# Optimization experiments

Measured on AMD Instinct MI355X. Metric: run time of the kernel, lower is better.

The kernel has to match this reference:

```python
import jax, jax.numpy as jnp
import numpy as np

N_NODES = 100000
N_EDGES = 3200000
IN_DIM = 512
OUT_DIM = 3


def _sage_conv(x, src, dst, ll_w, ll_b, lr_w):
    # PyG SAGEConv (mean aggr): out = lin_l(mean_{j in N(i)} x_j) + lin_r(x_i)
    n = x.shape[0]
    msgs = x[src]                                            # [E, d_in]
    agg = jax.ops.segment_sum(msgs, dst, num_segments=n)      # [N, d_in]
    cnt = jax.ops.segment_sum(jnp.ones((src.shape[0],), x.dtype), dst, num_segments=n)
    mean = agg / jnp.maximum(cnt, 1.0)[:, None]
    return mean @ ll_w + ll_b + x @ lr_w


def setup_inputs() -> dict:
    key = jax.random.key(0)
    ks = jax.random.split(key, 16)
    d = {}
    d["x"] = jax.random.normal(ks[0], (N_NODES, IN_DIM), dtype=jnp.float32)
    d["edge_index"] = jax.random.randint(ks[1], (2, N_EDGES), 0, N_NODES, dtype=jnp.int64)
    s = lambda fan_in: 1.0 / np.sqrt(fan_in)
    d["fc1_w"] = jax.random.uniform(ks[2], (IN_DIM, 16), jnp.float32, -s(IN_DIM), s(IN_DIM))
    d["fc1_b"] = jax.random.uniform(ks[3], (16,), jnp.float32, -s(IN_DIM), s(IN_DIM))
    d["conv1_ll_w"] = jax.random.uniform(ks[4], (16, 32), jnp.float32, -s(16), s(16))
    d["conv1_ll_b"] = jnp.zeros((32,), jnp.float32)
    d["conv1_lr_w"] = jax.random.uniform(ks[5], (16, 32), jnp.float32, -s(16), s(16))
    d["conv2_ll_w"] = jax.random.uniform(ks[6], (32, 16), jnp.float32, -s(32), s(32))
    d["conv2_ll_b"] = jnp.zeros((16,), jnp.float32)
    d["conv2_lr_w"] = jax.random.uniform(ks[7], (32, 16), jnp.float32, -s(32), s(32))
    d["fc2_w"] = jax.random.uniform(ks[8], (16, OUT_DIM), jnp.float32, -s(16), s(16))
    d["fc2_b"] = jax.random.uniform(ks[9], (OUT_DIM,), jnp.float32, -s(16), s(16))
    return d


def reference(x, edge_index, fc1_w, fc1_b, conv1_ll_w, conv1_ll_b, conv1_lr_w,
              conv2_ll_w, conv2_ll_b, conv2_lr_w, fc2_w, fc2_b):
    src, dst = edge_index[0], edge_index[1]
    h = jax.nn.relu(x @ fc1_w + fc1_b)                              # [N, 16]
    h = jax.nn.relu(_sage_conv(h, src, dst, conv1_ll_w, conv1_ll_b, conv1_lr_w))  # [N, 32]
    h = jax.nn.relu(_sage_conv(h, src, dst, conv2_ll_w, conv2_ll_b, conv2_lr_w))  # [N, 16]
    h = h @ fc2_w + fc2_b                                           # [N, 3]
    gsi = jax.nn.sigmoid(h[:, 1])
    mxi = jax.nn.sigmoid(h[:, 2])
    fsi = jax.nn.relu(h[:, 0]) + gsi
    return jnp.stack([fsi, gsi, mxi], axis=1)
```

## Files before the change

### kernel.cpp

```cpp
#include <hip/hip_runtime.h>
#include <math.h>

#define N_NODES 100000
#define N_EDGES 3200000
#define BSHIFT 8
#define NPB 256
#define BMASK (NPB - 1)
#define NB 391
#define CAP 10240
#define STG_BLOCKS 512
#define FC1_BLOCKS 2048
#define NTILES 6250
#define STG_PER 6252

typedef __attribute__((ext_vector_type(8))) short short8v;
typedef __attribute__((ext_vector_type(4))) float f32x4;
typedef __attribute__((address_space(3))) unsigned lds_u32;
typedef const __attribute__((address_space(1))) unsigned glb_u32;

__device__ inline unsigned cvt_pk_bf16(float a, float b) {
  unsigned r;
  asm("v_cvt_pk_bf16_f32 %0, %1, %2" : "=v"(r) : "v"(a), "v"(b));
  return r;
}
__device__ inline unsigned short f32_to_bf16(float f) {
  union { float f; unsigned u; } v; v.f = f;
  unsigned r = v.u + 0x7fff + ((v.u >> 16) & 1);
  return (unsigned short)(r >> 16);
}
__device__ inline float bf16_to_f32(unsigned short h) {
  union { unsigned u; float f; } v; v.u = ((unsigned)h) << 16;
  return v.f;
}

__global__ __launch_bounds__(256) void fc1_stage_kernel(
    const float* __restrict__ x, const float* __restrict__ w,
    const float* __restrict__ b, unsigned short* __restrict__ h1,
    const int* __restrict__ src, const int* __restrict__ dst,
    int* __restrict__ gcur, int* __restrict__ staged) {
  __shared__ __align__(16) char smem[53248];

  if (blockIdx.x >= STG_BLOCKS) {
    float* tile = (float*)smem;
    short8v (*wlds)[64] = (short8v(*)[64])(smem + 32768);
    f32x4* pbuf = (f32x4*)(smem + 49152);
    const int tid = threadIdx.x;
    const int lane = tid & 63;
    const int wib = tid >> 6;
    const int o = lane & 15;
    const int kb = lane >> 4;

    for (int i = tid; i < 2048; i += 256)
      ((float4*)tile)[i] = ((const float4*)w)[i];
    __syncthreads();
    for (int idx = tid; idx < 4096; idx += 256) {
      const int s = idx >> 8, ln = (idx >> 2) & 63, j = idx & 3;
      const int lkb = ln >> 4, lo = ln & 15;
      const int k = s * 32 + lkb * 8 + 2 * j;
      ((unsigned*)&wlds[s][ln])[j] =
          cvt_pk_bf16(tile[k * 16 + lo], tile[(k + 1) * 16 + lo]);
    }
    __syncthreads();

    const float bias = b[o];
    const int fcb = blockIdx.x - STG_BLOCKS;

    for (int tileid = fcb; tileid < NTILES; tileid += FC1_BLOCKS) {
      const float* xbase = x + (size_t)tileid * 8192;
#pragma unroll
      for (int i = 0; i < 8; ++i) {
        const int c = wib * 8 + i;
        const int r = c >> 1;
        const int off = (c & 1) * 1024 + lane * 16;
        const int goff = off ^ ((r & 7) << 5);
        __builtin_amdgcn_global_load_lds(
            (glb_u32*)(xbase + r * 512 + (goff >> 2)),
            (lds_u32*)((char*)tile + (size_t)c * 1024 + lane * 16) - lane * 4,
            16, 0, 0);
      }
      __syncthreads();

      f32x4 c4 = {0.f, 0.f, 0.f, 0.f};
#pragma unroll
      for (int ss = 0; ss < 4; ++ss) {
        const int s = wib * 4 + ss;
        const int cb = (s * 128 + kb * 32) ^ ((o & 7) << 5);
        const char* p = (const char*)tile + o * 2048 + cb;
        const float4 a0 = *(const float4*)p;
        const float4 a1 = *(const float4*)(p + 16);
        union { unsigned u[4]; short8v v; } fa;
        fa.u[0] = cvt_pk_bf16(a0.x, a0.y);
        fa.u[1] = cvt_pk_bf16(a0.z, a0.w);
        fa.u[2] = cvt_pk_bf16(a1.x, a1.y);
        fa.u[3] = cvt_pk_bf16(a1.z, a1.w);
        c4 = __builtin_amdgcn_mfma_f32_16x16x32_bf16(fa.v, wlds[s][lane], c4,
                                                     0, 0, 0);
      }
      pbuf[wib * 64 + lane] = c4;
      __syncthreads();
      if (wib == 0) {
        const f32x4 p0 = pbuf[lane];
        const f32x4 p1 = pbuf[64 + lane];
        const f32x4 p2 = pbuf[128 + lane];
        const f32x4 p3 = pbuf[192 + lane];
        const int rbase = tileid * 16 + (lane >> 4) * 4;
#pragma unroll
        for (int j = 0; j < 4; ++j) {
          const float vj = (p0[j] + p1[j]) + (p2[j] + p3[j]);
          h1[(size_t)(rbase + j) * 16 + o] =
              f32_to_bf16(fmaxf(vj + bias, 0.f));
        }
      }
      __syncthreads();
    }
  } else {
    int* hist = (int*)smem;
    int* base = (int*)(smem + 2048);
    const int tid = threadIdx.x;
    for (int i = tid; i < NB; i += 256) hist[i] = 0;
    __syncthreads();

    const int sb = blockIdx.x;
    const int e0 = sb * STG_PER;
    const int e1 = min(e0 + STG_PER, N_EDGES);
    const int em = e0 + ((e1 - e0) & ~3);

    for (int e = e0 + tid * 4; e < em; e += 1024) {
      const int4 d4 = *(const int4*)(dst + e);
      atomicAdd(&hist[d4.x >> BSHIFT], 1);
      atomicAdd(&hist[d4.y >> BSHIFT], 1);
      atomicAdd(&hist[d4.z >> BSHIFT], 1);
      atomicAdd(&hist[d4.w >> BSHIFT], 1);
    }
    for (int e = em + tid; e < e1; e += 256) {
      atomicAdd(&hist[dst[e] >> BSHIFT], 1);
    }
    __syncthreads();
    for (int bkt = tid; bkt < NB; bkt += 256) {
      int h = hist[bkt];
      base[bkt] = (h > 0) ? atomicAdd(&gcur[bkt], h) : 0;
      hist[bkt] = 0;
    }
    __syncthreads();
    for (int e = e0 + tid * 4; e < em; e += 1024) {
      const int4 d4 = *(const int4*)(dst + e);
      const int4 s4 = *(const int4*)(src + e);
      int bkt, pos;
      bkt = d4.x >> BSHIFT;
      pos = base[bkt] + atomicAdd(&hist[bkt], 1);
      if (pos < CAP) staged[bkt * CAP + pos] = (s4.x << 8) | (d4.x & BMASK);
      bkt = d4.y >> BSHIFT;
      pos = base[bkt] + atomicAdd(&hist[bkt], 1);
      if (pos < CAP) staged[bkt * CAP + pos] = (s4.y << 8) | (d4.y & BMASK);
      bkt = d4.z >> BSHIFT;
      pos = base[bkt] + atomicAdd(&hist[bkt], 1);
      if (pos < CAP) staged[bkt * CAP + pos] = (s4.z << 8) | (d4.z & BMASK);
      bkt = d4.w >> BSHIFT;
      pos = base[bkt] + atomicAdd(&hist[bkt], 1);
      if (pos < CAP) staged[bkt * CAP + pos] = (s4.w << 8) | (d4.w & BMASK);
    }
    for (int e = em + tid; e < e1; e += 256) {
      const int d = dst[e];
      const int s = src[e];
      const int bkt = d >> BSHIFT;
      const int pos = base[bkt] + atomicAdd(&hist[bkt], 1);
      if (pos < CAP) staged[bkt * CAP + pos] = (s << 8) | (d & BMASK);
    }
  }
}

__global__ __launch_bounds__(256) void finalize_kernel(
    int* __restrict__ staged, const int* __restrict__ gcur,
    int* __restrict__ offs, int* __restrict__ cnt) {
  __shared__ int ed[CAP];
  __shared__ int lcnt[NPB];
  __shared__ int lofs[NPB];
  __shared__ int sc[256];
  const int bkt = blockIdx.x, tid = threadIdx.x;
  const int nE = min(gcur[bkt], CAP);
  const int base = bkt * CAP;
  for (int e = tid; e < nE; e += 256) ed[e] = staged[base + e];
  lcnt[tid] = 0;
  __syncthreads();
  for (int e = tid; e < nE; e += 256) atomicAdd(&lcnt[ed[e] & BMASK], 1);
  __syncthreads();
  const int v = lcnt[tid];
  sc[tid] = v;
  __syncthreads();
  for (int d = 1; d < 256; d <<= 1) {
    int add = (tid >= d) ? sc[tid - d] : 0;
    __syncthreads();
    sc[tid] += add;
    __syncthreads();
  }
  const int excl = sc[tid] - v;
  lofs[tid] = excl;
  const int g = bkt * NPB + tid;
  if (g < N_NODES) {
    offs[g] = base + excl;
    cnt[g] = v;
  }
  lcnt[tid] = 0;
  __syncthreads();
  for (int e = tid; e < nE; e += 256) {
    int u = ed[e];
    int dl = u & BMASK;
    int pos = lofs[dl] + atomicAdd(&lcnt[dl], 1);
    staged[base + pos] = u >> 8;
  }
}

__global__ __launch_bounds__(256) void conv1_kernel(
    const unsigned short* __restrict__ h1, const int* __restrict__ csr,
    const int* __restrict__ offs, const int* __restrict__ cnt,
    const float* __restrict__ llw, const float* __restrict__ llb,
    const float* __restrict__ lrw, const float* __restrict__ c2llw,
    float* __restrict__ h2, unsigned short* __restrict__ t2) {
  __shared__ float wl[512], wr[512], w2c[512];
  __shared__ float bb[32];
  for (int idx = threadIdx.x; idx < 512; idx += 256) {
    const int k = idx >> 5, jj = idx & 31;
    const int sj = 4 * ((jj >> 2) ^ (k >> 2)) + (jj & 3);
    wl[k * 32 + sj] = llw[idx];
    wr[k * 32 + sj] = lrw[idx];
    w2c[idx] = c2llw[idx];
  }
  if (threadIdx.x < 32) bb[threadIdx.x] = llb[threadIdx.x];
  __syncthreads();

  const int tid = blockIdx.x * 256 + threadIdx.x;
  const int i = tid >> 3;
  if (i >= N_NODES) return;
  const int t8 = threadIdx.x & 7;
  const int gg = t8 >> 2;
  const int t = t8 & 3;
  const int start = offs[i], deg = cnt[i];

  float4 acc = make_float4(0.f, 0.f, 0.f, 0.f);
  int e = gg;
  for (; e + 6 < deg; e += 8) {
    const int s0 = csr[start + e];
    const int s1 = csr[start + e + 2];
    const int s2 = csr[start + e + 4];
    const int s3 = csr[start + e + 6];
    ushort4 a0 = *(const ushort4*)(h1 + (size_t)s0 * 16 + t * 4);
    ushort4 a1 = *(const ushort4*)(h1 + (size_t)s1 * 16 + t * 4);
    ushort4 a2 = *(const ushort4*)(h1 + (size_t)s2 * 16 + t * 4);
    ushort4 a3 = *(const ushort4*)(h1 + (size_t)s3 * 16 + t * 4);
    acc.x += (bf16_to_f32(a0.x) + bf16_to_f32(a1.x)) +
             (bf16_to_f32(a2.x) + bf16_to_f32(a3.x));
    acc.y += (bf16_to_f32(a0.y) + bf16_to_f32(a1.y)) +
             (bf16_to_f32(a2.y) + bf16_to_f32(a3.y));
    acc.z += (bf16_to_f32(a0.z) + bf16_to_f32(a1.z)) +
             (bf16_to_f32(a2.z) + bf16_to_f32(a3.z));
    acc.w += (bf16_to_f32(a0.w) + bf16_to_f32(a1.w)) +
             (bf16_to_f32(a2.w) + bf16_to_f32(a3.w));
  }
  for (; e < deg; e += 2) {
    const int s = csr[start + e];
    ushort4 a = *(const ushort4*)(h1 + (size_t)s * 16 + t * 4);
    acc.x += bf16_to_f32(a.x); acc.y += bf16_to_f32(a.y);
    acc.z += bf16_to_f32(a.z); acc.w += bf16_to_f32(a.w);
  }
  acc.x += __shfl_xor(acc.x, 4, 64);
  acc.y += __shfl_xor(acc.y, 4, 64);
  acc.z += __shfl_xor(acc.z, 4, 64);
  acc.w += __shfl_xor(acc.w, 4, 64);

  const float inv = 1.f / (float)(deg > 0 ? deg : 1);
  const ushort4 selfu = *(const ushort4*)(h1 + (size_t)i * 16 + t * 4);
  const float mk[4] = {acc.x * inv, acc.y * inv, acc.z * inv, acc.w * inv};
  const float sk[4] = {bf16_to_f32(selfu.x), bf16_to_f32(selfu.y),
                       bf16_to_f32(selfu.z), bf16_to_f32(selfu.w)};

  float4 p[8];
#pragma unroll
  for (int q = 0; q < 8; ++q) p[q] = make_float4(0.f, 0.f, 0.f, 0.f);
#pragma unroll
  for (int j = 0; j < 4; ++j) {
    const int k = 4 * t + j;
#pragma unroll
    for (int q = 0; q < 8; ++q) {
      const int qs = 4 * (q ^ t);
      float4 w4l = *(const float4*)&wl[k * 32 + qs];
      float4 w4r = *(const float4*)&wr[k * 32 + qs];
      p[q].x += mk[j] * w4l.x + sk[j] * w4r.x;
      p[q].y += mk[j] * w4l.y + sk[j] * w4r.y;
      p[q].z += mk[j] * w4l.z + sk[j] * w4r.z;
      p[q].w += mk[j] * w4l.w + sk[j] * w4r.w;
    }
  }
#pragma unroll
  for (int mask = 1; mask <= 2; mask <<= 1) {
#pragma unroll
    for (int q = 0; q < 8; ++q) {
      p[q].x += __shfl_xor(p[q].x, mask, 64);
      p[q].y += __shfl_xor(p[q].y, mask, 64);
      p[q].z += __shfl_xor(p[q].z, mask, 64);
      p[q].w += __shfl_xor(p[q].w, mask, 64);
    }
  }
  float o[32];
#pragma unroll
  for (int q = 0; q < 8; ++q) {
    o[4 * q + 0] = fmaxf(p[q].x + bb[4 * q + 0], 0.f);
    o[4 * q + 1] = fmaxf(p[q].y + bb[4 * q + 1], 0.f);
    o[4 * q + 2] = fmaxf(p[q].z + bb[4 * q + 2], 0.f);
    o[4 * q + 3] = fmaxf(p[q].w + bb[4 * q + 3], 0.f);
  }
  *(float4*)(h2 + (size_t)i * 32 + 4 * t8) =
      make_float4(o[4 * t8], o[4 * t8 + 1], o[4 * t8 + 2], o[4 * t8 + 3]);
  float t0 = 0.f, t1 = 0.f;
#pragma unroll
  for (int k = 0; k < 32; ++k) {
    const float ok = o[k];
    t0 += ok * w2c[k * 16 + 2 * t8];
    t1 += ok * w2c[k * 16 + 2 * t8 + 1];
  }
  *(unsigned*)(t2 + (size_t)i * 16 + 2 * t8) = cvt_pk_bf16(t0, t1);
}

__global__ __launch_bounds__(256) void conv2_kernel(
    const unsigned short* __restrict__ t2, const float* __restrict__ h2,
    const int* __restrict__ csr, const int* __restrict__ offs,
    const int* __restrict__ cnt, const float* __restrict__ llb,
    const float* __restrict__ lrw, const float* __restrict__ fc2w,
    const float* __restrict__ fc2b, float* __restrict__ out) {
  __shared__ float wr[512];
  __shared__ float bb[16];
  __shared__ float w2[48];
  __shared__ float b2[3];
  for (int idx = threadIdx.x; idx < 512; idx += 256) {
    const int k = idx >> 4, jj = idx & 15;
    const int sj = 4 * ((jj >> 2) ^ ((k >> 2) & 3)) + (jj & 3);
    wr[k * 16 + sj] = lrw[idx];
  }
  if (threadIdx.x < 16) bb[threadIdx.x] = llb[threadIdx.x];
  else if (threadIdx.x >= 64 && threadIdx.x < 112) w2[threadIdx.x - 64] = fc2w[threadIdx.x - 64];
  else if (threadIdx.x >= 128 && threadIdx.x < 131) b2[threadIdx.x - 128] = fc2b[threadIdx.x - 128];
  __syncthreads();

  const int tid = blockIdx.x * 256 + threadIdx.x;
  const int i = tid >> 3;
  if (i >= N_NODES) return;
  const int t8 = threadIdx.x & 7;
  const int gg = t8 >> 2;
  const int t = t8 & 3;
  const int start = offs[i], deg = cnt[i];

  float4 acc = make_float4(0.f, 0.f, 0.f, 0.f);
  int e = gg;
  for (; e + 6 < deg; e += 8) {
    const int s0 = csr[start + e];
    const int s1 = csr[start + e + 2];
    const int s2 = csr[start + e + 4];
    const int s3 = csr[start + e + 6];
    ushort4 a0 = *(const ushort4*)(t2 + (size_t)s0 * 16 + t * 4);
    ushort4 a1 = *(const ushort4*)(t2 + (size_t)s1 * 16 + t * 4);
    ushort4 a2 = *(const ushort4*)(t2 + (size_t)s2 * 16 + t * 4);
    ushort4 a3 = *(const ushort4*)(t2 + (size_t)s3 * 16 + t * 4);
    acc.x += (bf16_to_f32(a0.x) + bf16_to_f32(a1.x)) +
             (bf16_to_f32(a2.x) + bf16_to_f32(a3.x));
    acc.y += (bf16_to_f32(a0.y) + bf16_to_f32(a1.y)) +
             (bf16_to_f32(a2.y) + bf16_to_f32(a3.y));
    acc.z += (bf16_to_f32(a0.z) + bf16_to_f32(a1.z)) +
             (bf16_to_f32(a2.z) + bf16_to_f32(a3.z));
    acc.w += (bf16_to_f32(a0.w) + bf16_to_f32(a1.w)) +
             (bf16_to_f32(a2.w) + bf16_to_f32(a3.w));
  }
  for (; e < deg; e += 2) {
    const int s = csr[start + e];
    ushort4 a = *(const ushort4*)(t2 + (size_t)s * 16 + t * 4);
    acc.x += bf16_to_f32(a.x); acc.y += bf16_to_f32(a.y);
    acc.z += bf16_to_f32(a.z); acc.w += bf16_to_f32(a.w);
  }
  acc.x += __shfl_xor(acc.x, 4, 64);
  acc.y += __shfl_xor(acc.y, 4, 64);
  acc.z += __shfl_xor(acc.z, 4, 64);
  acc.w += __shfl_xor(acc.w, 4, 64);

  const float inv = 1.f / (float)(deg > 0 ? deg : 1);
  const float4 s0v = *(const float4*)(h2 + (size_t)i * 32 + 4 * t8);
  const float sk[4] = {s0v.x, s0v.y, s0v.z, s0v.w};
  float4 p[4];
#pragma unroll
  for (int q = 0; q < 4; ++q) p[q] = make_float4(0.f, 0.f, 0.f, 0.f);
#pragma unroll
  for (int kk = 0; kk < 4; ++kk) {
    const int k = 4 * t8 + kk;
    const float s = sk[kk];
#pragma unroll
    for (int q = 0; q < 4; ++q) {
      const int qs = 4 * (q ^ (t8 & 3));
      const float4 wv = *(const float4*)&wr[k * 16 + qs];
      p[q].x += s * wv.x; p[q].y += s * wv.y;
      p[q].z += s * wv.z; p[q].w += s * wv.w;
    }
  }
  if (gg == 0) {
    p[t].x += acc.x * inv; p[t].y += acc.y * inv;
    p[t].z += acc.z * inv; p[t].w += acc.w * inv;
  }
#pragma unroll
  for (int mask = 1; mask <= 4; mask <<= 1) {
#pragma unroll
    for (int q = 0; q < 4; ++q) {
      p[q].x += __shfl_xor(p[q].x, mask, 64);
      p[q].y += __shfl_xor(p[q].y, mask, 64);
      p[q].z += __shfl_xor(p[q].z, mask, 64);
      p[q].w += __shfl_xor(p[q].w, mask, 64);
    }
  }
  if (t8 < 3) {
    float f[16];
#pragma unroll
    for (int q = 0; q < 4; ++q) {
      f[4 * q + 0] = fmaxf(p[q].x + bb[4 * q + 0], 0.f);
      f[4 * q + 1] = fmaxf(p[q].y + bb[4 * q + 1], 0.f);
      f[4 * q + 2] = fmaxf(p[q].z + bb[4 * q + 2], 0.f);
      f[4 * q + 3] = fmaxf(p[q].w + bb[4 * q + 3], 0.f);
    }
    float v0 = b2[0], v1 = b2[1], v2 = b2[2];
#pragma unroll
    for (int k = 0; k < 16; ++k) {
      v0 += f[k] * w2[k * 3 + 0];
      v1 += f[k] * w2[k * 3 + 1];
      v2 += f[k] * w2[k * 3 + 2];
    }
    float gsi = 1.f / (1.f + expf(-v1));
    float mxi = 1.f / (1.f + expf(-v2));
    float fsi = fmaxf(v0, 0.f) + gsi;
    float rv = (t8 == 0) ? fsi : ((t8 == 1) ? gsi : mxi);
    out[(size_t)i * 3 + t8] = rv;
  }
}

extern "C" void kernel_launch(void* const* d_in, const int* in_sizes, int n_in,
                              void* d_out, int out_size, void* d_ws, size_t ws_size,
                              hipStream_t stream) {
  const float* x = (const float*)d_in[0];
  const int* ei = (const int*)d_in[1];
  const float* fc1w = (const float*)d_in[2];
  const float* fc1b = (const float*)d_in[3];
  const float* c1llw = (const float*)d_in[4];
  const float* c1llb = (const float*)d_in[5];
  const float* c1lrw = (const float*)d_in[6];
  const float* c2llw = (const float*)d_in[7];
  const float* c2llb = (const float*)d_in[8];
  const float* c2lrw = (const float*)d_in[9];
  const float* fc2w = (const float*)d_in[10];
  const float* fc2b = (const float*)d_in[11];
  float* outp = (float*)d_out;
  const int* src = ei;
  const int* dst = ei + N_EDGES;

  char* ws = (char*)d_ws;
  unsigned short* h1 = (unsigned short*)ws;  ws += (size_t)N_NODES * 16 * 2;
  float* h2 = (float*)ws;                    ws += (size_t)N_NODES * 32 * 4;
  unsigned short* t2 = (unsigned short*)ws;  ws += (size_t)N_NODES * 16 * 2;
  int* staged = (int*)ws;                    ws += (size_t)NB * CAP * 4;
  int* gcur = (int*)ws;                      ws += (size_t)NB * 4;
  int* offs = (int*)ws;                      ws += (size_t)N_NODES * 4;
  int* cnt = (int*)ws;                       ws += (size_t)N_NODES * 4;
  (void)ws_size; (void)n_in; (void)in_sizes; (void)out_size;

  hipMemsetAsync(gcur, 0, (size_t)NB * 4, stream);
  fc1_stage_kernel<<<STG_BLOCKS + FC1_BLOCKS, 256, 0, stream>>>(
      x, fc1w, fc1b, h1, src, dst, gcur, staged);
  finalize_kernel<<<NB, 256, 0, stream>>>(staged, gcur, offs, cnt);
  conv1_kernel<<<(N_NODES * 8 + 255) / 256, 256, 0, stream>>>(
      h1, staged, offs, cnt, c1llw, c1llb, c1lrw, c2llw, h2, t2);
  conv2_kernel<<<(N_NODES * 8 + 255) / 256, 256, 0, stream>>>(
      t2, h2, staged, offs, cnt, c2llb, c2lrw, fc2w, fc2b, outp);
}
```

Baseline: 212.9 us.

## Double-buffer fc1 x tiles in LDS to overlap global loads with MFMA

Each 16x512 fc1 input tile is now split into two 256-column halves loaded into alternating LDS buffers, with the next half issued before the current half is computed. Manual vmcnt waits and raw s_barriers replace full syncthreads. The goal is to hide global-to-LDS load latency behind MFMA compute in this memory-bound fc1 stage. The cost is trickier synchronisation and a risk of race conditions between buffer reuse and the pbuf reduction. Weight staging is also reordered through registers so the weight scratch area can overlap the tile buffers.

```diff
diff --git a/kernel.cpp b/kernel.cpp
--- a/kernel.cpp
+++ b/kernel.cpp
@@ -33,6 +33,37 @@
   return v.f;
 }
 
+#define ISSUE(tl, ch, bufsel)                                              \
+  {                                                                        \
+    const float* xb_ = x + (size_t)(tl) * 8192 + (ch) * 256;               \
+    char* dst_ = smem + (bufsel) * 16384;                                  \
+    _Pragma("unroll") for (int i_ = 0; i_ < 4; ++i_) {                     \
+      const int r_ = wib * 4 + i_;                                         \
+      const int gb_ = (lane * 16) ^ ((r_ & 7) << 5);                       \
+      __builtin_amdgcn_global_load_lds(                                    \
+          (glb_u32*)(xb_ + r_ * 512 + (gb_ >> 2)),                         \
+          (lds_u32*)(dst_ + r_ * 1024), 16, 0, 0);                         \
+    }                                                                      \
+  }
+#define COMPUTE(ch, bufsel)                                                \
+  {                                                                        \
+    const char* bb_ = smem + (bufsel) * 16384;                             \
+    _Pragma("unroll") for (int u_ = 0; u_ < 2; ++u_) {                     \
+      const int ls_ = wib * 2 + u_;                                        \
+      const int cb_ = (ls_ * 128 + kb * 32) ^ ((o & 7) << 5);              \
+      const char* p_ = bb_ + o * 1024 + cb_;                               \
+      const float4 a0_ = *(const float4*)p_;                               \
+      const float4 a1_ = *(const float4*)(p_ + 16);                        \
+      union { unsigned u[4]; short8v v; } fa_;                             \
+      fa_.u[0] = cvt_pk_bf16(a0_.x, a0_.y);                                \
+      fa_.u[1] = cvt_pk_bf16(a0_.z, a0_.w);                                \
+      fa_.u[2] = cvt_pk_bf16(a1_.x, a1_.y);                                \
+      fa_.u[3] = cvt_pk_bf16(a1_.z, a1_.w);                                \
+      c4 = __builtin_amdgcn_mfma_f32_16x16x32_bf16(                        \
+          fa_.v, wlds[(ch) * 8 + ls_][lane], c4, 0, 0, 0);                 \
+    }                                                                      \
+  }
+
 __global__ __launch_bounds__(256) void fc1_stage_kernel(
     const float* __restrict__ x, const float* __restrict__ w,
     const float* __restrict__ b, unsigned short* __restrict__ h1,
@@ -41,7 +72,6 @@
   __shared__ __align__(16) char smem[53248];
 
   if (blockIdx.x >= STG_BLOCKS) {
-    float* tile = (float*)smem;
     short8v (*wlds)[64] = (short8v(*)[64])(smem + 32768);
     f32x4* pbuf = (f32x4*)(smem + 49152);
     const int tid = threadIdx.x;
@@ -50,60 +80,57 @@
     const int o = lane & 15;
     const int kb = lane >> 4;
 
+    float* scratch = (float*)smem;
     for (int i = tid; i < 2048; i += 256)
-      ((float4*)tile)[i] = ((const float4*)w)[i];
-    __syncthreads();
-    for (int idx = tid; idx < 4096; idx += 256) {
+      ((float4*)scratch)[i] = ((const float4*)w)[i];
+    __syncthreads();
+    unsigned wpk[16];
+    for (int idx = tid, n = 0; idx < 4096; idx += 256, ++n) {
       const int s = idx >> 8, ln = (idx >> 2) & 63, j = idx & 3;
       const int lkb = ln >> 4, lo = ln & 15;
       const int k = s * 32 + lkb * 8 + 2 * j;
-      ((unsigned*)&wlds[s][ln])[j] =
-          cvt_pk_bf16(tile[k * 16 + lo], tile[(k + 1) * 16 + lo]);
+      wpk[n] = cvt_pk_bf16(scratch[k * 16 + lo], scratch[(k + 1) * 16 + lo]);
+    }
+    __syncthreads();
+    for (int idx = tid, n = 0; idx < 4096; idx += 256, ++n) {
+      ((unsigned*)wlds)[idx] = wpk[n];
     }
     __syncthreads();
 
     const float bias = b[o];
     const int fcb = blockIdx.x - STG_BLOCKS;
-
-    for (int tileid = fcb; tileid < NTILES; tileid += FC1_BLOCKS) {
-      const float* xbase = x + (size_t)tileid * 8192;
-#pragma unroll
-      for (int i = 0; i < 8; ++i) {
-        const int c = wib * 8 + i;
-        const int r = c >> 1;
-        const int off = (c & 1) * 1024 + lane * 16;
-        const int goff = off ^ ((r & 7) << 5);
-        __builtin_amdgcn_global_load_lds(
-            (glb_u32*)(xbase + r * 512 + (goff >> 2)),
-            (lds_u32*)((char*)tile + (size_t)c * 1024 + lane * 16) - lane * 4,
-            16, 0, 0);
+    int cur = 0;
+    int t = fcb;
+    if (t < NTILES) ISSUE(t, 0, cur);
+
+    for (; t < NTILES; t += FC1_BLOCKS) {
+      f32x4 c4 = {0.f, 0.f, 0.f, 0.f};
+      ISSUE(t, 1, 1 - cur);
+      asm volatile("s_waitcnt vmcnt(4)" ::: "memory");
+      __builtin_amdgcn_sched_barrier(0);
+      __builtin_amdgcn_s_barrier();
+      COMPUTE(0, cur);
+      __builtin_amdgcn_s_barrier();
+      cur ^= 1;
+      const int tn = t + FC1_BLOCKS;
+      if (tn < NTILES) {
+        ISSUE(tn, 0, 1 - cur);
+        asm volatile("s_waitcnt vmcnt(4)" ::: "memory");
+      } else {
+        asm volatile("s_waitcnt vmcnt(0)" ::: "memory");
       }
-      __syncthreads();
-
-      f32x4 c4 = {0.f, 0.f, 0.f, 0.f};
-#pragma unroll
-      for (int ss = 0; ss < 4; ++ss) {
-        const int s = wib * 4 + ss;
-        const int cb = (s * 128 + kb * 32) ^ ((o & 7) << 5);
-        const char* p = (const char*)tile + o * 2048 + cb;
-        const float4 a0 = *(const float4*)p;
-        const float4 a1 = *(const float4*)(p + 16);
-        union { unsigned u[4]; short8v v; } fa;
-        fa.u[0] = cvt_pk_bf16(a0.x, a0.y);
-        fa.u[1] = cvt_pk_bf16(a0.z, a0.w);
-        fa.u[2] = cvt_pk_bf16(a1.x, a1.y);
-        fa.u[3] = cvt_pk_bf16(a1.z, a1.w);
-        c4 = __builtin_amdgcn_mfma_f32_16x16x32_bf16(fa.v, wlds[s][lane], c4,
-                                                     0, 0, 0);
-      }
+      __builtin_amdgcn_sched_barrier(0);
+      __builtin_amdgcn_s_barrier();
+      COMPUTE(1, cur);
       pbuf[wib * 64 + lane] = c4;
-      __syncthreads();
+      asm volatile("s_waitcnt lgkmcnt(0)" ::: "memory");
+      __builtin_amdgcn_s_barrier();
       if (wib == 0) {
         const f32x4 p0 = pbuf[lane];
         const f32x4 p1 = pbuf[64 + lane];
         const f32x4 p2 = pbuf[128 + lane];
         const f32x4 p3 = pbuf[192 + lane];
-        const int rbase = tileid * 16 + (lane >> 4) * 4;
+        const int rbase = t * 16 + (lane >> 4) * 4;
 #pragma unroll
         for (int j = 0; j < 4; ++j) {
           const float vj = (p0[j] + p1[j]) + (p2[j] + p3[j]);
@@ -111,7 +138,7 @@
               f32_to_bf16(fmaxf(vj + bias, 0.f));
         }
       }
-      __syncthreads();
+      cur ^= 1;
     }
   } else {
     int* hist = (int*)smem;
```

Result: no change. 214.8 us (+0.9%).
